# Optimization experiments

Measured on AMD Instinct MI355X. Metric: run time of the kernel, lower is better.

## Reference

```python
import jax, jax.numpy as jnp
import numpy as np
from jax import lax

B, N, F_IN, DIM = 128, 200, 200, 32
E_PER = 6400
K1, K2 = 100, 50
OUT = 2
BN_EPS = 1e-5


def setup_inputs():
    key = jax.random.key(0)
    ks = jax.random.split(key, 16)
    x = jax.random.normal(ks[0], (B * N, F_IN), jnp.float32)
    src = jax.random.randint(ks[1], (B, E_PER), 0, N)
    dst = jax.random.randint(ks[2], (B, E_PER), 0, N)
    off = (jnp.arange(B) * N)[:, None]
    edge_index = jnp.stack([(src + off).reshape(-1), (dst + off).reshape(-1)]).astype(jnp.int32)
    batch = jnp.repeat(jnp.arange(B, dtype=jnp.int32), N)

    def lin(k, i, o):
        kw, kb = jax.random.split(k)
        return (jax.random.normal(kw, (i, o), jnp.float32) / np.float32(np.sqrt(i)),
                jax.random.normal(kb, (o,), jnp.float32) * 0.01)

    w1a, b1a = lin(ks[3], F_IN, DIM)
    w1b, b1b = lin(ks[4], DIM, DIM)
    w2a, b2a = lin(ks[5], DIM, DIM)
    w2b, b2b = lin(ks[6], DIM, DIM)
    pw1 = jax.random.normal(ks[7], (DIM,), jnp.float32)
    pw2 = jax.random.normal(ks[8], (DIM,), jnp.float32)
    fc1_w, fc1_b = lin(ks[9], 2 * DIM, 4 * DIM)
    fc2_w, fc2_b = lin(ks[10], 4 * DIM, 8 * DIM)
    fc3_w, fc3_b = lin(ks[11], 8 * DIM, OUT)
    return dict(x=x, edge_index=edge_index, batch=batch,
                w1a=w1a, b1a=b1a, w1b=w1b, b1b=b1b,
                w2a=w2a, b2a=b2a, w2b=w2b, b2b=b2b,
                pw1=pw1, pw2=pw2,
                fc1_w=fc1_w, fc1_b=fc1_b, fc2_w=fc2_w, fc2_b=fc2_b,
                fc3_w=fc3_w, fc3_b=fc3_b,
                bn1_g=jnp.ones((4 * DIM,)), bn1_b=jnp.zeros((4 * DIM,)),
                bn1_m=jnp.zeros((4 * DIM,)), bn1_v=jnp.ones((4 * DIM,)),
                bn2_g=jnp.ones((8 * DIM,)), bn2_b=jnp.zeros((8 * DIM,)),
                bn2_m=jnp.zeros((8 * DIM,)), bn2_v=jnp.ones((8 * DIM,)))


def gin_conv(x, src, dst, valid, wa, ba, wb, bb, n_nodes):
    # PyG GINConv: mlp((1+eps)*x + sum_{j->i} x_j), eps=0 (default)
    msg = x[src]
    if valid is not None:
        msg = msg * valid[:, None]
    aggr = jax.ops.segment_sum(msg, dst, num_segments=n_nodes)
    h = jax.nn.relu((x + aggr) @ wa + ba)
    return h @ wb + bb


def topk_pool(x, src, dst, valid, pw, nb, n_per, k):
    # PyG TopKPooling: score = tanh((x.w)/||w||); keep top-k per graph; x <- x[perm]*score[perm]
    score = jnp.tanh((x @ pw) / jnp.linalg.norm(pw))
    topv, topi = lax.top_k(score.reshape(nb, n_per), k)  # [nb,k], descending (matches PyG ordering)
    perm = (topi + (jnp.arange(nb) * n_per)[:, None]).reshape(-1)
    x_new = x[perm] * topv.reshape(-1, 1)
    new_id = jnp.full((nb * n_per,), -1, jnp.int32).at[perm].set(jnp.arange(nb * k, dtype=jnp.int32))
    s, d = new_id[src], new_id[dst]
    v = (s >= 0) & (d >= 0)
    if valid is not None:
        v = v & valid
    return x_new, jnp.maximum(s, 0), jnp.maximum(d, 0), v, topv


def bn_eval(h, g, b, m, v):
    return (h - m) * lax.rsqrt(v + BN_EPS) * g + b


def reference(x, edge_index, batch,
              w1a, b1a, w1b, b1b, w2a, b2a, w2b, b2b, pw1, pw2,
              fc1_w, fc1_b, fc2_w, fc2_b, fc3_w, fc3_b,
              bn1_g, bn1_b, bn1_m, bn1_v, bn2_g, bn2_b, bn2_m, bn2_v):
    src, dst = edge_index[0], edge_index[1]
    h = jax.nn.relu(gin_conv(x, src, dst, None, w1a, b1a, w1b, b1b, B * N))
    h, src, dst, valid, attn1 = topk_pool(h, src, dst, None, pw1, B, N, K1)
    hb = h.reshape(B, K1, DIM)
    x1 = jnp.concatenate([hb.max(axis=1), hb.mean(axis=1)], axis=1)  # gmp || gap
    h = jax.nn.relu(gin_conv(h, src, dst, valid.astype(h.dtype), w2a, b2a, w2b, b2b, B * K1))
    h, src, dst, valid, attn2 = topk_pool(h, src, dst, valid, pw2, B, K1, K2)
    hb = h.reshape(B, K2, DIM)
    x2 = jnp.concatenate([hb.max(axis=1), hb.mean(axis=1)], axis=1)
    z = x1 + x2
    z = bn_eval(jax.nn.relu(z @ fc1_w + fc1_b), bn1_g, bn1_b, bn1_m, bn1_v)  # dropout p=0.6 inactive (eval)
    z = bn_eval(jax.nn.relu(z @ fc2_w + fc2_b), bn2_g, bn2_b, bn2_m, bn2_v)
    xy = jax.nn.log_softmax(z @ fc3_w + fc3_b, axis=-1)
    return xy, jax.nn.sigmoid(attn1), jax.nn.sigmoid(attn2)
```

## Files before the change

kernel.cpp:

```cpp
#include <hip/hip_runtime.h>
#include <math.h>

#define NGRAPH 128
#define NNODE  200
#define FIN    200
#define DIM    32
#define EPER   6400
#define ETOT   819200
#define KP1    100
#define KP2    50

#define W1B_OFF  0
#define W2A_OFF  1024
#define W2B_OFF  2048
#define B1A_OFF  3072
#define B1B_OFF  3104
#define B2A_OFF  3136
#define B2B_OFF  3168
#define PW1_OFF  3200
#define PW2_OFF  3232
#define NRM1_OFF 3264
#define NRM2_OFF 3265
#define SW_SIZE  3280

__device__ __forceinline__ int swz(int row, int chunk) {
  return (row << 5) + (((chunk ^ ((row >> 2) & 7))) << 2);
}

__global__ __launch_bounds__(256, 2) void proj_k(const float* __restrict__ x,
                                                 const float* __restrict__ w1a,
                                                 float* __restrict__ y) {
  __shared__ __align__(16) float sw[FIN * DIM];
  const int tid = threadIdx.x;
  for (int i = tid; i < FIN * DIM; i += 256) sw[i] = w1a[i];
  __syncthreads();
  if (tid >= 200) return;
  const int rg = tid >> 2, cg = tid & 3;
  const int d0 = cg * 8;
  const int r0 = blockIdx.x * 50 + rg;
  const float* x0 = x + (size_t)r0 * FIN;
  float a0[8] = {0, 0, 0, 0, 0, 0, 0, 0};
  for (int k = 0; k < FIN; k += 4) {
    const float4 xa = *(const float4*)&x0[k];
#pragma unroll
    for (int j = 0; j < 4; ++j) {
      const float4 wa = *(const float4*)&sw[(k + j) * DIM + d0];
      const float4 wb = *(const float4*)&sw[(k + j) * DIM + d0 + 4];
      const float s0 = (j == 0) ? xa.x : (j == 1) ? xa.y : (j == 2) ? xa.z : xa.w;
      a0[0] += s0 * wa.x; a0[1] += s0 * wa.y; a0[2] += s0 * wa.z; a0[3] += s0 * wa.w;
      a0[4] += s0 * wb.x; a0[5] += s0 * wb.y; a0[6] += s0 * wb.z; a0[7] += s0 * wb.w;
    }
  }
  float4 o;
  o.x = a0[0]; o.y = a0[1]; o.z = a0[2]; o.w = a0[3];
  *(float4*)&y[(size_t)r0 * 32 + d0] = o;
  o.x = a0[4]; o.y = a0[5]; o.z = a0[6]; o.w = a0[7];
  *(float4*)&y[(size_t)r0 * 32 + d0 + 4] = o;
}

template <int ROWS, bool RELU, bool BIAS, bool FUSE>
__device__ __forceinline__ void mm2r(const float* __restrict__ A,
                                     const float* __restrict__ A2,
                                     const float* __restrict__ fb,
                                     const float* __restrict__ W,
                                     float* __restrict__ O,
                                     const float* __restrict__ bias, int tid) {
  if (tid < ROWS * 2) {
    const int rg = tid >> 2, cg = tid & 3;
    const int r0 = rg * 2, d0 = cg * 8;
    float acc[2][8];
#pragma unroll
    for (int r = 0; r < 2; ++r)
#pragma unroll
      for (int c = 0; c < 8; ++c) acc[r][c] = 0.f;
#pragma unroll
    for (int kc = 0; kc < 8; ++kc) {
      float4 av[2];
#pragma unroll
      for (int r = 0; r < 2; ++r) {
        const int p = swz(r0 + r, kc);
        float4 v = *(const float4*)&A[p];
        if (FUSE) {
          const float4 u = *(const float4*)&A2[p];
          const float4 b = *(const float4*)&fb[kc * 4];
          v.x = fmaxf(v.x + u.x + b.x, 0.f);
          v.y = fmaxf(v.y + u.y + b.y, 0.f);
          v.z = fmaxf(v.z + u.z + b.z, 0.f);
          v.w = fmaxf(v.w + u.w + b.w, 0.f);
        }
        av[r] = v;
      }
#pragma unroll
      for (int j = 0; j < 4; ++j) {
        const int k = kc * 4 + j;
        const float4 wa = *(const float4*)&W[k * 32 + d0];
        const float4 wb = *(const float4*)&W[k * 32 + d0 + 4];
#pragma unroll
        for (int r = 0; r < 2; ++r) {
          const float xs = (j == 0) ? av[r].x : (j == 1) ? av[r].y
                                  : (j == 2) ? av[r].z : av[r].w;
          acc[r][0] += xs * wa.x; acc[r][1] += xs * wa.y;
          acc[r][2] += xs * wa.z; acc[r][3] += xs * wa.w;
          acc[r][4] += xs * wb.x; acc[r][5] += xs * wb.y;
          acc[r][6] += xs * wb.z; acc[r][7] += xs * wb.w;
        }
      }
    }
#pragma unroll
    for (int r = 0; r < 2; ++r) {
      float v[8];
#pragma unroll
      for (int c = 0; c < 8; ++c) {
        float t = acc[r][c];
        if (BIAS) t += bias[d0 + c];
        if (RELU) t = fmaxf(t, 0.f);
        v[c] = t;
      }
      float4 o0, o1;
      o0.x = v[0]; o0.y = v[1]; o0.z = v[2]; o0.w = v[3];
      o1.x = v[4]; o1.y = v[5]; o1.z = v[6]; o1.w = v[7];
      *(float4*)&O[swz(r0 + r, cg * 2)] = o0;
      *(float4*)&O[swz(r0 + r, cg * 2 + 1)] = o1;
    }
  }
}

__device__ __forceinline__ void scan_counts(const int* __restrict__ cnt,
                                            int* __restrict__ start, int lane) {
  const int b = lane * 4;
  const int c0 = (cnt[b + 0] + 3) & ~3;
  const int c1 = (cnt[b + 1] + 3) & ~3;
  const int c2 = (cnt[b + 2] + 3) & ~3;
  const int c3 = (cnt[b + 3] + 3) & ~3;
  const int t01 = c0 + c1;
  const int t012 = t01 + c2;
  const int tot = t012 + c3;
  int run = tot;
#pragma unroll
  for (int off = 1; off < 64; off <<= 1) {
    const int t = __shfl_up(run, off);
    if (lane >= off) run += t;
  }
  const int e = run - tot;
  start[b + 0] = e;
  start[b + 1] = e + c0;
  start[b + 2] = e + t01;
  start[b + 3] = e + t012;
}

template <int NN>
__device__ __forceinline__ void aggregate(const float* __restrict__ sYv,
                                          float* __restrict__ sAgv,
                                          const int* __restrict__ sSrcv,
                                          const int* __restrict__ sStartv,
                                          const int* __restrict__ sCntv, int tid) {
  const int slot = tid >> 3, part = tid & 7;
#pragma unroll
  for (int p = 0; p < (NN + 127) / 128; ++p) {
    const int n = p * 128 + slot;
    if (n < NN) {
      const int jb = sStartv[n];
      const int je = jb + sCntv[n];
      float4 a0 = {0, 0, 0, 0}, a1 = {0, 0, 0, 0}, a2 = {0, 0, 0, 0}, a3 = {0, 0, 0, 0};
      int j = jb;
      for (; j + 4 <= je; j += 4) {
        const int4 ss = *(const int4*)&sSrcv[j];
        const float4 v0 = *(const float4*)&sYv[swz(ss.x, part)];
        const float4 v1 = *(const float4*)&sYv[swz(ss.y, part)];
        const float4 v2 = *(const float4*)&sYv[swz(ss.z, part)];
        const float4 v3 = *(const float4*)&sYv[swz(ss.w, part)];
        a0.x += v0.x; a0.y += v0.y; a0.z += v0.z; a0.w += v0.w;
        a1.x += v1.x; a1.y += v1.y; a1.z += v1.z; a1.w += v1.w;
        a2.x += v2.x; a2.y += v2.y; a2.z += v2.z; a2.w += v2.w;
        a3.x += v3.x; a3.y += v3.y; a3.z += v3.z; a3.w += v3.w;
      }
      for (; j < je; ++j) {
        const float4 v = *(const float4*)&sYv[swz(sSrcv[j], part)];
        a0.x += v.x; a0.y += v.y; a0.z += v.z; a0.w += v.w;
      }
      float4 o;
      o.x = (a0.x + a1.x) + (a2.x + a3.x);
      o.y = (a0.y + a1.y) + (a2.y + a3.y);
      o.z = (a0.z + a1.z) + (a2.z + a3.z);
      o.w = (a0.w + a1.w) + (a2.w + a3.w);
      *(float4*)&sAgv[swz(n, part)] = o;
    }
  }
}

__global__ __launch_bounds__(1024, 1) void gin_rest(
    const float* __restrict__ y1g_all, const int* __restrict__ ei,
    const float* __restrict__ b1a, const float* __restrict__ w1b,
    const float* __restrict__ b1b, const float* __restrict__ w2a,
    const float* __restrict__ b2a, const float* __restrict__ w2b,
    const float* __restrict__ b2b, const float* __restrict__ pw1,
    const float* __restrict__ pw2,
    const float* __restrict__ fc1w, const float* __restrict__ fc1b,
    const float* __restrict__ fc2w, const float* __restrict__ fc2b,
    const float* __restrict__ fc3w, const float* __restrict__ fc3b,
    const float* __restrict__ bn1g, const float* __restrict__ bn1b,
    const float* __restrict__ bn1m, const float* __restrict__ bn1v,
    const float* __restrict__ bn2g, const float* __restrict__ bn2b,
    const float* __restrict__ bn2m, const float* __restrict__ bn2v,
    float* __restrict__ out) {
  __shared__ __align__(16) float sY[6400];
  __shared__ __align__(16) float sAg[6400];
  __shared__ __align__(16) float sH[6400];
  __shared__ __align__(16) float sHp[3200];
  __shared__ __align__(16) float sW[SW_SIZE];
  __shared__ __align__(16) int sSrc[7040];
  __shared__ unsigned short sEdge[6400];
  __shared__ int sCnt[256], sStart[256], sOfs[256];
  __shared__ int sCnt2[256], sStart2[256], sOfs2[256];
  __shared__ float sScore[256];
  __shared__ int sNewid[256];
  __shared__ float sZ[64];
  __shared__ float sZ1[128];
  __shared__ float sZ2[256];
  __shared__ float sLg[2];

  const int tid = threadIdx.x;
  const int g = blockIdx.x;

  if (tid < 512) {
    if (tid < 256) { sCnt[tid] = 0; sOfs[tid] = 0; }
    const float* yg = y1g_all + (size_t)g * (NNODE * DIM);
    for (int i = tid; i < 1600; i += 512) {
      const float4 v = *(const float4*)&yg[i * 4];
      *(float4*)&sY[swz(i >> 3, i & 7)] = v;
    }
    for (int i = tid; i < 1024; i += 512) {
      sW[W1B_OFF + i] = w1b[i];
      sW[W2A_OFF + i] = w2a[i];
      sW[W2B_OFF + i] = w2b[i];
    }
    if (tid < 32) {
      sW[B1A_OFF + tid] = b1a[tid];
      sW[B1B_OFF + tid] = b1b[tid];
      sW[B2A_OFF + tid] = b2a[tid];
      sW[B2B_OFF + tid] = b2b[tid];
      sW[PW1_OFF + tid] = pw1[tid];
      sW[PW2_OFF + tid] = pw2[tid];
    }
  } else {
    const int eb = g * EPER, nb = g * NNODE;
    for (int i = tid - 512; i < EPER / 4; i += 512) {
      const int4 ss = *(const int4*)&ei[eb + i * 4];
      const int4 dd = *(const int4*)&ei[ETOT + eb + i * 4];
      sEdge[i * 4 + 0] = (unsigned short)(((ss.x - nb) << 8) | (dd.x - nb));
      sEdge[i * 4 + 1] = (unsigned short)(((ss.y - nb) << 8) | (dd.y - nb));
      sEdge[i * 4 + 2] = (unsigned short)(((ss.z - nb) << 8) | (dd.z - nb));
      sEdge[i * 4 + 3] = (unsigned short)(((ss.w - nb) << 8) | (dd.w - nb));
    }
  }
  __syncthreads();

  if (tid == 0) {
    float s = 0.f;
    for (int k = 0; k < 32; ++k) s += sW[PW1_OFF + k] * sW[PW1_OFF + k];
    sW[NRM1_OFF] = sqrtf(s);
  } else if (tid == 1) {
    float s = 0.f;
    for (int k = 0; k < 32; ++k) s += sW[PW2_OFF + k] * sW[PW2_OFF + k];
    sW[NRM2_OFF] = sqrtf(s);
  }
  if (tid < 800) {
    const uint4 u = *(const uint4*)&sEdge[tid * 8];
    atomicAdd(&sCnt[u.x & 255], 1);
    atomicAdd(&sCnt[(u.x >> 16) & 255], 1);
    atomicAdd(&sCnt[u.y & 255], 1);
    atomicAdd(&sCnt[(u.y >> 16) & 255], 1);
    atomicAdd(&sCnt[u.z & 255], 1);
    atomicAdd(&sCnt[(u.z >> 16) & 255], 1);
    atomicAdd(&sCnt[u.w & 255], 1);
    atomicAdd(&sCnt[(u.w >> 16) & 255], 1);
  }
  __syncthreads();

  if (tid < 64) scan_counts(sCnt, sStart, tid);
  __syncthreads();

  for (int e = tid; e < EPER; e += 1024) {
    const unsigned short p = sEdge[e];
    sSrc[sStart[p & 255] + atomicAdd(&sOfs[p & 255], 1)] = p >> 8;
  }
  __syncthreads();

  aggregate<NNODE>(sY, sAg, sSrc, sStart, sCnt, tid);
  __syncthreads();

  mm2r<200, true, true, true>(sY, sAg, &sW[B1A_OFF], &sW[W1B_OFF], sH,
                              &sW[B1B_OFF], tid);
  if (tid >= 512) {
    const int i = tid - 512;
    if (i < 256) sCnt2[i] = 0;
    else if (i < 512) sOfs2[i - 256] = 0;
  }
  __syncthreads();

  if (tid < NNODE) {
    float dot = 0.f;
#pragma unroll
    for (int kc = 0; kc < 8; ++kc) {
      const float4 v = *(const float4*)&sH[swz(tid, kc)];
      const float4 w = *(const float4*)&sW[PW1_OFF + kc * 4];
      dot += v.x * w.x + v.y * w.y + v.z * w.z + v.w * w.w;
    }
    sScore[tid] = tanhf(dot / sW[NRM1_OFF]);
  }
  __syncthreads();

  if (tid < NNODE * 4) {
    const int n = tid >> 2, q = tid & 3;
    const float s = sScore[n];
    int r = 0;
    for (int m = q * 50; m < q * 50 + 50; ++m) {
      const float sm = sScore[m];
      r += (sm > s) || (sm == s && m < n);
    }
    r += __shfl_xor(r, 1);
    r += __shfl_xor(r, 2);
    if (q == 0) {
      sNewid[n] = (r < KP1) ? r : -1;
      if (r < KP1) out[2 * NGRAPH + g * KP1 + r] = 1.f / (1.f + expf(-s));
    }
  }
  __syncthreads();

  if (tid < 400) {
    const int n = tid >> 1, kb = (tid & 1) * 4;
    const int r = sNewid[n];
    if (r >= 0) {
      const float sc = sScore[n];
#pragma unroll
      for (int k = 0; k < 4; ++k) {
        float4 v = *(const float4*)&sH[swz(n, kb + k)];
        v.x *= sc; v.y *= sc; v.z *= sc; v.w *= sc;
        *(float4*)&sHp[swz(r, kb + k)] = v;
      }
    }
  } else if (tid >= 512) {
    for (int e = tid - 512; e < EPER; e += 512) {
      const unsigned short p = sEdge[e];
      const int s1 = sNewid[p >> 8], d1 = sNewid[p & 255];
      if (s1 >= 0 && d1 >= 0) atomicAdd(&sCnt2[d1], 1);
    }
  }
  __syncthreads();

  if (tid < 32) {
    const int ch = tid >> 2, w = tid & 3;
    float m0 = -INFINITY, m1 = -INFINITY, s0 = 0.f, s1 = 0.f;
    for (int r = 0; r < KP1; r += 2) {
      const float v0 = sHp[swz(r, ch) + w];
      const float v1 = sHp[swz(r + 1, ch) + w];
      m0 = fmaxf(m0, v0); m1 = fmaxf(m1, v1);
      s0 += v0; s1 += v1;
    }
    sZ[tid] = fmaxf(m0, m1);
    sZ[32 + tid] = (s0 + s1) / (float)KP1;
  } else if (tid >= 64 && tid < 128) {
    scan_counts(sCnt2, sStart2, tid - 64);
  }
  __syncthreads();

  mm2r<KP1, false, false, false>(sHp, nullptr, nullptr, &sW[W2A_OFF], sY,
                                 nullptr, tid);
  if (tid >= 256) {
    for (int e = tid - 256; e < EPER; e += 768) {
      const unsigned short p = sEdge[e];
      const int s1 = sNewid[p >> 8], d1 = sNewid[p & 255];
      if (s1 >= 0 && d1 >= 0)
        sSrc[sStart2[d1] + atomicAdd(&sOfs2[d1], 1)] = s1;
    }
  }
  __syncthreads();

  aggregate<KP1>(sY, sAg, sSrc, sStart2, sCnt2, tid);
  __syncthreads();

  mm2r<KP1, true, true, true>(sY, sAg, &sW[B2A_OFF], &sW[W2B_OFF], sH,
                              &sW[B2B_OFF], tid);
  __syncthreads();

  if (tid < KP1) {
    float dot = 0.f;
#pragma unroll
    for (int kc = 0; kc < 8; ++kc) {
      const float4 v = *(const float4*)&sH[swz(tid, kc)];
      const float4 w = *(const float4*)&sW[PW2_OFF + kc * 4];
      dot += v.x * w.x + v.y * w.y + v.z * w.z + v.w * w.w;
    }
    sScore[tid] = tanhf(dot / sW[NRM2_OFF]);
  }
  __syncthreads();

  if (tid < KP1 * 4) {
    const int n = tid >> 2, q = tid & 3;
    const float s = sScore[n];
    int r = 0;
    for (int m = q * 25; m < q * 25 + 25; ++m) {
      const float sm = sScore[m];
      r += (sm > s) || (sm == s && m < n);
    }
    r += __shfl_xor(r, 1);
    r += __shfl_xor(r, 2);
    if (q == 0) {
      sNewid[n] = (r < KP2) ? r : -1;
      if (r < KP2)
        out[2 * NGRAPH + NGRAPH * KP1 + g * KP2 + r] = 1.f / (1.f + expf(-s));
    }
  }
  __syncthreads();

  if (tid < 200) {
    const int n = tid >> 1, kb = (tid & 1) * 4;
    const int r = sNewid[n];
    if (r >= 0) {
      const float sc = sScore[n];
#pragma unroll
      for (int k = 0; k < 4; ++k) {
        float4 v = *(const float4*)&sH[swz(n, kb + k)];
        v.x *= sc; v.y *= sc; v.z *= sc; v.w *= sc;
        *(float4*)&sHp[swz(r, kb + k)] = v;
      }
    }
  }
  __syncthreads();

  if (tid < 32) {
    const int ch = tid >> 2, w = tid & 3;
    float m0 = -INFINITY, m1 = -INFINITY, s0 = 0.f, s1 = 0.f;
    for (int r = 0; r < KP2; r += 2) {
      const float v0 = sHp[swz(r, ch) + w];
      const float v1 = sHp[swz(r + 1, ch) + w];
      m0 = fmaxf(m0, v0); m1 = fmaxf(m1, v1);
      s0 += v0; s1 += v1;
    }
    sZ[tid] += fmaxf(m0, m1);
    sZ[32 + tid] += (s0 + s1) / (float)KP2;
  }
  __syncthreads();

  if (tid < 128) {
    float a = fc1b[tid];
    for (int k = 0; k < 64; ++k) a += sZ[k] * fc1w[k * 128 + tid];
    a = fmaxf(a, 0.f);
    a = (a - bn1m[tid]) * rsqrtf(bn1v[tid] + 1e-5f) * bn1g[tid] + bn1b[tid];
    sZ1[tid] = a;
  }
  __syncthreads();

  if (tid < 256) {
    float a = fc2b[tid];
    for (int k = 0; k < 128; ++k) a += sZ1[k] * fc2w[k * 256 + tid];
    a = fmaxf(a, 0.f);
    a = (a - bn2m[tid]) * rsqrtf(bn2v[tid] + 1e-5f) * bn2g[tid] + bn2b[tid];
    sZ2[tid] = a;
  }
  __syncthreads();

  if (tid < 128) {
    const int o = tid >> 6, lane = tid & 63;
    float a = 0.f;
    for (int k = lane; k < 256; k += 64) a += sZ2[k] * fc3w[k * 2 + o];
#pragma unroll
    for (int off = 32; off; off >>= 1) a += __shfl_down(a, off);
    if (lane == 0) sLg[o] = a + fc3b[o];
  }
  __syncthreads();

  if (tid == 0) {
    const float l0 = sLg[0], l1 = sLg[1];
    const float m = fmaxf(l0, l1);
    const float lse = m + logf(expf(l0 - m) + expf(l1 - m));
    out[g * 2 + 0] = l0 - lse;
    out[g * 2 + 1] = l1 - lse;
  }
}

extern "C" void kernel_launch(void* const* d_in, const int* in_sizes, int n_in,
                              void* d_out, int out_size, void* d_ws,
                              size_t ws_size, hipStream_t stream) {
  (void)in_sizes; (void)n_in; (void)out_size; (void)ws_size;
  float* y1 = (float*)d_ws;
  proj_k<<<512, 256, 0, stream>>>((const float*)d_in[0],
                                  (const float*)d_in[3], y1);
  gin_rest<<<NGRAPH, 1024, 0, stream>>>(
      y1, (const int*)d_in[1],
      (const float*)d_in[4],
      (const float*)d_in[5], (const float*)d_in[6],
      (const float*)d_in[7], (const float*)d_in[8],
      (const float*)d_in[9], (const float*)d_in[10],
      (const float*)d_in[11], (const float*)d_in[12],
      (const float*)d_in[13], (const float*)d_in[14],
      (const float*)d_in[15], (const float*)d_in[16],
      (const float*)d_in[17], (const float*)d_in[18],
      (const float*)d_in[19], (const float*)d_in[20],
      (const float*)d_in[21], (const float*)d_in[22],
      (const float*)d_in[23], (const float*)d_in[24],
      (const float*)d_in[25], (const float*)d_in[26],
      (float*)d_out);
}
```

Before: 52.21 us.

## Fuse input projection into per-graph kernel and overlap edge sorting via LDS flags

```diff
diff --git a/kernel.cpp b/kernel.cpp
--- a/kernel.cpp
+++ b/kernel.cpp
@@ -27,44 +27,20 @@
   return (row << 5) + (((chunk ^ ((row >> 2) & 7))) << 2);
 }
 
-__global__ __launch_bounds__(256, 2) void proj_k(const float* __restrict__ x,
-                                                 const float* __restrict__ w1a,
-                                                 float* __restrict__ y) {
-  __shared__ __align__(16) float sw[FIN * DIM];
-  const int tid = threadIdx.x;
-  for (int i = tid; i < FIN * DIM; i += 256) sw[i] = w1a[i];
-  __syncthreads();
-  if (tid >= 200) return;
-  const int rg = tid >> 2, cg = tid & 3;
-  const int d0 = cg * 8;
-  const int r0 = blockIdx.x * 50 + rg;
-  const float* x0 = x + (size_t)r0 * FIN;
-  float a0[8] = {0, 0, 0, 0, 0, 0, 0, 0};
-  for (int k = 0; k < FIN; k += 4) {
-    const float4 xa = *(const float4*)&x0[k];
-#pragma unroll
-    for (int j = 0; j < 4; ++j) {
-      const float4 wa = *(const float4*)&sw[(k + j) * DIM + d0];
-      const float4 wb = *(const float4*)&sw[(k + j) * DIM + d0 + 4];
-      const float s0 = (j == 0) ? xa.x : (j == 1) ? xa.y : (j == 2) ? xa.z : xa.w;
-      a0[0] += s0 * wa.x; a0[1] += s0 * wa.y; a0[2] += s0 * wa.z; a0[3] += s0 * wa.w;
-      a0[4] += s0 * wb.x; a0[5] += s0 * wb.y; a0[6] += s0 * wb.z; a0[7] += s0 * wb.w;
-    }
-  }
-  float4 o;
-  o.x = a0[0]; o.y = a0[1]; o.z = a0[2]; o.w = a0[3];
-  *(float4*)&y[(size_t)r0 * 32 + d0] = o;
-  o.x = a0[4]; o.y = a0[5]; o.z = a0[6]; o.w = a0[7];
-  *(float4*)&y[(size_t)r0 * 32 + d0 + 4] = o;
-}
-
-template <int ROWS, bool RELU, bool BIAS, bool FUSE>
+__device__ __forceinline__ void lds_spin(volatile int* f, int target) {
+  while (*f != target) __builtin_amdgcn_s_sleep(2);
+}
+
+template <int ROWS, bool RELU, bool BIAS, bool FUSE, bool SCORE>
 __device__ __forceinline__ void mm2r(const float* __restrict__ A,
                                      const float* __restrict__ A2,
                                      const float* __restrict__ fb,
                                      const float* __restrict__ W,
                                      float* __restrict__ O,
-                                     const float* __restrict__ bias, int tid) {
+                                     const float* __restrict__ bias,
+                                     const float* __restrict__ pw,
+                                     const float* __restrict__ nrmp,
+                                     float* __restrict__ scoreOut, int tid) {
   if (tid < ROWS * 2) {
     const int rg = tid >> 2, cg = tid & 3;
     const int r0 = rg * 2, d0 = cg * 8;
@@ -106,6 +82,7 @@
         }
       }
     }
+    float dot[2] = {0.f, 0.f};
 #pragma unroll
     for (int r = 0; r < 2; ++r) {
       float v[8];
@@ -116,11 +93,26 @@
         if (RELU) t = fmaxf(t, 0.f);
         v[c] = t;
       }
+      if (SCORE) {
+        float d = 0.f;
+#pragma unroll
+        for (int c = 0; c < 8; ++c) d += v[c] * pw[d0 + c];
+        dot[r] = d;
+      }
       float4 o0, o1;
       o0.x = v[0]; o0.y = v[1]; o0.z = v[2]; o0.w = v[3];
       o1.x = v[4]; o1.y = v[5]; o1.z = v[6]; o1.w = v[7];
       *(float4*)&O[swz(r0 + r, cg * 2)] = o0;
       *(float4*)&O[swz(r0 + r, cg * 2 + 1)] = o1;
+    }
+    if (SCORE) {
+      dot[0] += __shfl_xor(dot[0], 1); dot[0] += __shfl_xor(dot[0], 2);
+      dot[1] += __shfl_xor(dot[1], 1); dot[1] += __shfl_xor(dot[1], 2);
+      if ((tid & 3) == 0) {
+        const float nrm = *nrmp;
+        scoreOut[r0] = tanhf(dot[0] / nrm);
+        scoreOut[r0 + 1] = tanhf(dot[1] / nrm);
+      }
     }
   }
 }
@@ -188,13 +180,13 @@
   }
 }
 
-__global__ __launch_bounds__(1024, 1) void gin_rest(
-    const float* __restrict__ y1g_all, const int* __restrict__ ei,
-    const float* __restrict__ b1a, const float* __restrict__ w1b,
-    const float* __restrict__ b1b, const float* __restrict__ w2a,
-    const float* __restrict__ b2a, const float* __restrict__ w2b,
-    const float* __restrict__ b2b, const float* __restrict__ pw1,
-    const float* __restrict__ pw2,
+__global__ __launch_bounds__(1024, 1) void gin_fused(
+    const float* __restrict__ x, const int* __restrict__ ei,
+    const float* __restrict__ w1a, const float* __restrict__ b1a,
+    const float* __restrict__ w1b, const float* __restrict__ b1b,
+    const float* __restrict__ w2a, const float* __restrict__ b2a,
+    const float* __restrict__ w2b, const float* __restrict__ b2b,
+    const float* __restrict__ pw1, const float* __restrict__ pw2,
     const float* __restrict__ fc1w, const float* __restrict__ fc1b,
     const float* __restrict__ fc2w, const float* __restrict__ fc2b,
     const float* __restrict__ fc3w, const float* __restrict__ fc3b,
@@ -212,6 +204,7 @@
   __shared__ unsigned short sEdge[6400];
   __shared__ int sCnt[256], sStart[256], sOfs[256];
   __shared__ int sCnt2[256], sStart2[256], sOfs2[256];
+  __shared__ int sFlag[4];
   __shared__ float sScore[256];
   __shared__ int sNewid[256];
   __shared__ float sZ[64];
@@ -222,18 +215,9 @@
   const int tid = threadIdx.x;
   const int g = blockIdx.x;
 
-  if (tid < 512) {
-    if (tid < 256) { sCnt[tid] = 0; sOfs[tid] = 0; }
-    const float* yg = y1g_all + (size_t)g * (NNODE * DIM);
-    for (int i = tid; i < 1600; i += 512) {
-      const float4 v = *(const float4*)&yg[i * 4];
-      *(float4*)&sY[swz(i >> 3, i & 7)] = v;
-    }
-    for (int i = tid; i < 1024; i += 512) {
-      sW[W1B_OFF + i] = w1b[i];
-      sW[W2A_OFF + i] = w2a[i];
-      sW[W2B_OFF + i] = w2b[i];
-    }
+  if (tid < 256) {
+    for (int i = tid; i < 1600; i += 256)
+      *(float4*)&sAg[i * 4] = ((const float4*)w1a)[i];
     if (tid < 32) {
       sW[B1A_OFF + tid] = b1a[tid];
       sW[B1B_OFF + tid] = b1b[tid];
@@ -242,6 +226,21 @@
       sW[PW1_OFF + tid] = pw1[tid];
       sW[PW2_OFF + tid] = pw2[tid];
     }
+  } else if (tid < 512) {
+    const int t = tid - 256;
+    for (int i = t; i < 768; i += 256) {
+      const float4 v = (i < 256) ? ((const float4*)w1b)[i]
+                    : (i < 512) ? ((const float4*)w2a)[i - 256]
+                                : ((const float4*)w2b)[i - 512];
+      const int off = (i < 256) ? W1B_OFF + i * 4
+                    : (i < 512) ? W2A_OFF + (i - 256) * 4
+                                : W2B_OFF + (i - 512) * 4;
+      *(float4*)&sW[off] = v;
+    }
+    for (int i = t; i < 256; i += 256) {
+      sCnt[i] = 0; sOfs[i] = 0; sCnt2[i] = 0; sOfs2[i] = 0;
+    }
+    if (t < 4) sFlag[t] = 0;
   } else {
     const int eb = g * EPER, nb = g * NNODE;
     for (int i = tid - 512; i < EPER / 4; i += 512) {
@@ -255,59 +254,79 @@
   }
   __syncthreads();
 
-  if (tid == 0) {
+  if (tid < 200) {
+    const int rg = tid >> 2, cg = tid & 3;
+    const int n0 = rg * 4, d0 = cg * 8;
+    float acc[4][8];
+#pragma unroll
+    for (int r = 0; r < 4; ++r)
+#pragma unroll
+      for (int c = 0; c < 8; ++c) acc[r][c] = 0.f;
+    const float* xg = x + ((size_t)g * NNODE + n0) * FIN;
+    for (int k = 0; k < FIN; k += 4) {
+      float4 xv[4];
+#pragma unroll
+      for (int r = 0; r < 4; ++r)
+        xv[r] = *(const float4*)&xg[r * FIN + k];
+#pragma unroll
+      for (int j = 0; j < 4; ++j) {
+        const float4 wa = *(const float4*)&sAg[(k + j) * 32 + d0];
+        const float4 wb = *(const float4*)&sAg[(k + j) * 32 + d0 + 4];
+#pragma unroll
+        for (int r = 0; r < 4; ++r) {
+          const float xs = (j == 0) ? xv[r].x : (j == 1) ? xv[r].y
+                                   : (j == 2) ? xv[r].z : xv[r].w;
+          acc[r][0] += xs * wa.x; acc[r][1] += xs * wa.y;
+          acc[r][2] += xs * wa.z; acc[r][3] += xs * wa.w;
+          acc[r][4] += xs * wb.x; acc[r][5] += xs * wb.y;
+          acc[r][6] += xs * wb.z; acc[r][7] += xs * wb.w;
+        }
+      }
+    }
+#pragma unroll
+    for (int r = 0; r < 4; ++r) {
+      float4 o0, o1;
+      o0.x = acc[r][0]; o0.y = acc[r][1]; o0.z = acc[r][2]; o0.w = acc[r][3];
+      o1.x = acc[r][4]; o1.y = acc[r][5]; o1.z = acc[r][6]; o1.w = acc[r][7];
+      *(float4*)&sY[swz(n0 + r, cg * 2)] = o0;
+      *(float4*)&sY[swz(n0 + r, cg * 2 + 1)] = o1;
+    }
+  } else if (tid == 200) {
     float s = 0.f;
     for (int k = 0; k < 32; ++k) s += sW[PW1_OFF + k] * sW[PW1_OFF + k];
     sW[NRM1_OFF] = sqrtf(s);
-  } else if (tid == 1) {
+  } else if (tid == 201) {
     float s = 0.f;
     for (int k = 0; k < 32; ++k) s += sW[PW2_OFF + k] * sW[PW2_OFF + k];
     sW[NRM2_OFF] = sqrtf(s);
-  }
-  if (tid < 800) {
-    const uint4 u = *(const uint4*)&sEdge[tid * 8];
-    atomicAdd(&sCnt[u.x & 255], 1);
-    atomicAdd(&sCnt[(u.x >> 16) & 255], 1);
-    atomicAdd(&sCnt[u.y & 255], 1);
-    atomicAdd(&sCnt[(u.y >> 16) & 255], 1);
-    atomicAdd(&sCnt[u.z & 255], 1);
-    atomicAdd(&sCnt[(u.z >> 16) & 255], 1);
-    atomicAdd(&sCnt[u.w & 255], 1);
-    atomicAdd(&sCnt[(u.w >> 16) & 255], 1);
-  }
-  __syncthreads();
-
-  if (tid < 64) scan_counts(sCnt, sStart, tid);
-  __syncthreads();
-
-  for (int e = tid; e < EPER; e += 1024) {
-    const unsigned short p = sEdge[e];
-    sSrc[sStart[p & 255] + atomicAdd(&sOfs[p & 255], 1)] = p >> 8;
+  } else if (tid >= 256) {
+    const int t = tid - 256;
+    for (int e = t; e < EPER; e += 768)
+      atomicAdd(&sCnt[sEdge[e] & 255], 1);
+    __threadfence_block();
+    atomicAdd(&sFlag[0], 1);
+    if (tid >= 960) {
+      lds_spin(&sFlag[0], 768);
+      __threadfence_block();
+      scan_counts(sCnt, sStart, tid - 960);
+      __threadfence_block();
+      if (tid == 960) atomicExch(&sFlag[1], 1);
+    }
+    lds_spin(&sFlag[1], 1);
+    __threadfence_block();
+    for (int e = t; e < EPER; e += 768) {
+      const unsigned short p = sEdge[e];
+      sSrc[sStart[p & 255] + atomicAdd(&sOfs[p & 255], 1)] = p >> 8;
+    }
   }
   __syncthreads();
 
   aggregate<NNODE>(sY, sAg, sSrc, sStart, sCnt, tid);
   __syncthreads();
 
-  mm2r<200, true, true, true>(sY, sAg, &sW[B1A_OFF], &sW[W1B_OFF], sH,
-                              &sW[B1B_OFF], tid);
-  if (tid >= 512) {
-    const int i = tid - 512;
-    if (i < 256) sCnt2[i] = 0;
-    else if (i < 512) sOfs2[i - 256] = 0;
-  }
-  __syncthreads();
-
-  if (tid < NNODE) {
-    float dot = 0.f;
-#pragma unroll
-    for (int kc = 0; kc < 8; ++kc) {
-      const float4 v = *(const float4*)&sH[swz(tid, kc)];
-      const float4 w = *(const float4*)&sW[PW1_OFF + kc * 4];
-      dot += v.x * w.x + v.y * w.y + v.z * w.z + v.w * w.w;
-    }
-    sScore[tid] = tanhf(dot / sW[NRM1_OFF]);
-  }
+  mm2r<200, true, true, true, true>(sY, sAg, &sW[B1A_OFF], &sW[W1B_OFF], sH,
+                                    &sW[B1B_OFF], &sW[PW1_OFF], &sW[NRM1_OFF],
+                                    sScore, tid);
   __syncthreads();
 
   if (tid < NNODE * 4) {
@@ -324,32 +343,24 @@
       sNewid[n] = (r < KP1) ? r : -1;
       if (r < KP1) out[2 * NGRAPH + g * KP1 + r] = 1.f / (1.f + expf(-s));
     }
-  }
-  __syncthreads();
-
-  if (tid < 400) {
-    const int n = tid >> 1, kb = (tid & 1) * 4;
-    const int r = sNewid[n];
-    if (r >= 0) {
-      const float sc = sScore[n];
-#pragma unroll
-      for (int k = 0; k < 4; ++k) {
-        float4 v = *(const float4*)&sH[swz(n, kb + k)];
-        v.x *= sc; v.y *= sc; v.z *= sc; v.w *= sc;
-        *(float4*)&sHp[swz(r, kb + k)] = v;
-      }
-    }
-  } else if (tid >= 512) {
-    for (int e = tid - 512; e < EPER; e += 512) {
-      const unsigned short p = sEdge[e];
-      const int s1 = sNewid[p >> 8], d1 = sNewid[p & 255];
-      if (s1 >= 0 && d1 >= 0) atomicAdd(&sCnt2[d1], 1);
-    }
-  }
-  __syncthreads();
-
-  if (tid < 32) {
-    const int ch = tid >> 2, w = tid & 3;
+    if (r < KP1) {
+#pragma unroll
+      for (int c = 0; c < 2; ++c) {
+        const int ch = q * 2 + c;
+        float4 v = *(const float4*)&sH[swz(n, ch)];
+        v.x *= s; v.y *= s; v.z *= s; v.w *= s;
+        *(float4*)&sHp[swz(r, ch)] = v;
+      }
+    }
+  }
+  __syncthreads();
+
+  mm2r<KP1, false, false, false, false>(sHp, nullptr, nullptr, &sW[W2A_OFF],
+                                        sY, nullptr, nullptr, nullptr, nullptr,
+                                        tid);
+  if (tid >= 256 && tid < 288) {
+    const int t = tid - 256;
+    const int ch = t >> 2, w = t & 3;
     float m0 = -INFINITY, m1 = -INFINITY, s0 = 0.f, s1 = 0.f;
     for (int r = 0; r < KP1; r += 2) {
       const float v0 = sHp[swz(r, ch) + w];
@@ -357,17 +368,27 @@
       m0 = fmaxf(m0, v0); m1 = fmaxf(m1, v1);
       s0 += v0; s1 += v1;
     }
-    sZ[tid] = fmaxf(m0, m1);
-    sZ[32 + tid] = (s0 + s1) / (float)KP1;
-  } else if (tid >= 64 && tid < 128) {
-    scan_counts(sCnt2, sStart2, tid - 64);
-  }
-  __syncthreads();
-
-  mm2r<KP1, false, false, false>(sHp, nullptr, nullptr, &sW[W2A_OFF], sY,
-                                 nullptr, tid);
-  if (tid >= 256) {
-    for (int e = tid - 256; e < EPER; e += 768) {
+    sZ[t] = fmaxf(m0, m1);
+    sZ[32 + t] = (s0 + s1) / (float)KP1;
+  } else if (tid >= 512) {
+    const int t = tid - 512;
+    for (int e = t; e < EPER; e += 512) {
+      const unsigned short p = sEdge[e];
+      const int s1 = sNewid[p >> 8], d1 = sNewid[p & 255];
+      if (s1 >= 0 && d1 >= 0) atomicAdd(&sCnt2[d1], 1);
+    }
+    __threadfence_block();
+    atomicAdd(&sFlag[2], 1);
+    if (tid >= 960) {
+      lds_spin(&sFlag[2], 512);
+      __threadfence_block();
+      scan_counts(sCnt2, sStart2, tid - 960);
+      __threadfence_block();
+      if (tid == 960) atomicExch(&sFlag[3], 1);
+    }
+    lds_spin(&sFlag[3], 1);
+    __threadfence_block();
+    for (int e = t; e < EPER; e += 512) {
       const unsigned short p = sEdge[e];
       const int s1 = sNewid[p >> 8], d1 = sNewid[p & 255];
       if (s1 >= 0 && d1 >= 0)
@@ -379,20 +400,9 @@
   aggregate<KP1>(sY, sAg, sSrc, sStart2, sCnt2, tid);
   __syncthreads();
 
-  mm2r<KP1, true, true, true>(sY, sAg, &sW[B2A_OFF], &sW[W2B_OFF], sH,
-                              &sW[B2B_OFF], tid);
-  __syncthreads();
-
-  if (tid < KP1) {
-    float dot = 0.f;
-#pragma unroll
-    for (int kc = 0; kc < 8; ++kc) {
-      const float4 v = *(const float4*)&sH[swz(tid, kc)];
-      const float4 w = *(const float4*)&sW[PW2_OFF + kc * 4];
-      dot += v.x * w.x + v.y * w.y + v.z * w.z + v.w * w.w;
-    }
-    sScore[tid] = tanhf(dot / sW[NRM2_OFF]);
-  }
+  mm2r<KP1, true, true, true, true>(sY, sAg, &sW[B2A_OFF], &sW[W2B_OFF], sH,
+                                    &sW[B2B_OFF], &sW[PW2_OFF], &sW[NRM2_OFF],
+                                    sScore, tid);
   __syncthreads();
 
   if (tid < KP1 * 4) {
@@ -410,19 +420,13 @@
       if (r < KP2)
         out[2 * NGRAPH + NGRAPH * KP1 + g * KP2 + r] = 1.f / (1.f + expf(-s));
     }
-  }
-  __syncthreads();
-
-  if (tid < 200) {
-    const int n = tid >> 1, kb = (tid & 1) * 4;
-    const int r = sNewid[n];
-    if (r >= 0) {
-      const float sc = sScore[n];
-#pragma unroll
-      for (int k = 0; k < 4; ++k) {
-        float4 v = *(const float4*)&sH[swz(n, kb + k)];
-        v.x *= sc; v.y *= sc; v.z *= sc; v.w *= sc;
-        *(float4*)&sHp[swz(r, kb + k)] = v;
+    if (r < KP2) {
+#pragma unroll
+      for (int c = 0; c < 2; ++c) {
+        const int ch = q * 2 + c;
+        float4 v = *(const float4*)&sH[swz(n, ch)];
+        v.x *= s; v.y *= s; v.z *= s; v.w *= s;
+        *(float4*)&sHp[swz(r, ch)] = v;
       }
     }
   }
@@ -442,53 +446,66 @@
   }
   __syncthreads();
 
-  if (tid < 128) {
-    float a = fc1b[tid];
-    for (int k = 0; k < 64; ++k) a += sZ[k] * fc1w[k * 128 + tid];
-    a = fmaxf(a, 0.f);
-    a = (a - bn1m[tid]) * rsqrtf(bn1v[tid] + 1e-5f) * bn1g[tid] + bn1b[tid];
-    sZ1[tid] = a;
-  }
-  __syncthreads();
-
-  if (tid < 256) {
-    float a = fc2b[tid];
-    for (int k = 0; k < 128; ++k) a += sZ1[k] * fc2w[k * 256 + tid];
-    a = fmaxf(a, 0.f);
-    a = (a - bn2m[tid]) * rsqrtf(bn2v[tid] + 1e-5f) * bn2g[tid] + bn2b[tid];
-    sZ2[tid] = a;
-  }
-  __syncthreads();
-
-  if (tid < 128) {
-    const int o = tid >> 6, lane = tid & 63;
+  if (tid < 512) {
+    const int o = tid >> 2, q = tid & 3;
     float a = 0.f;
-    for (int k = lane; k < 256; k += 64) a += sZ2[k] * fc3w[k * 2 + o];
-#pragma unroll
-    for (int off = 32; off; off >>= 1) a += __shfl_down(a, off);
-    if (lane == 0) sLg[o] = a + fc3b[o];
-  }
-  __syncthreads();
-
-  if (tid == 0) {
-    const float l0 = sLg[0], l1 = sLg[1];
-    const float m = fmaxf(l0, l1);
-    const float lse = m + logf(expf(l0 - m) + expf(l1 - m));
-    out[g * 2 + 0] = l0 - lse;
-    out[g * 2 + 1] = l1 - lse;
+    for (int k = q * 16; k < q * 16 + 16; ++k) a += sZ[k] * fc1w[k * 128 + o];
+    a += __shfl_xor(a, 1);
+    a += __shfl_xor(a, 2);
+    if (q == 0) {
+      a += fc1b[o];
+      a = fmaxf(a, 0.f);
+      a = (a - bn1m[o]) * rsqrtf(bn1v[o] + 1e-5f) * bn1g[o] + bn1b[o];
+      sZ1[o] = a;
+    }
+  }
+  __syncthreads();
+
+  if (tid < 512) {
+    const int o = tid >> 1, h = tid & 1;
+    float a = 0.f;
+    for (int k = h * 64; k < h * 64 + 64; ++k) a += sZ1[k] * fc2w[k * 256 + o];
+    a += __shfl_xor(a, 1);
+    if (h == 0) {
+      a += fc2b[o];
+      a = fmaxf(a, 0.f);
+      a = (a - bn2m[o]) * rsqrtf(bn2v[o] + 1e-5f) * bn2g[o] + bn2b[o];
+      sZ2[o] = a;
+    }
+  }
+  __syncthreads();
+
+  if (tid < 64) {
+    const int k4 = tid * 4;
+    float a0 = 0.f, a1 = 0.f;
+#pragma unroll
+    for (int k = 0; k < 4; ++k) {
+      const float z = sZ2[k4 + k];
+      a0 += z * fc3w[(k4 + k) * 2 + 0];
+      a1 += z * fc3w[(k4 + k) * 2 + 1];
+    }
+#pragma unroll
+    for (int off = 32; off; off >>= 1) {
+      a0 += __shfl_xor(a0, off);
+      a1 += __shfl_xor(a1, off);
+    }
+    if (tid == 0) {
+      const float l0 = a0 + fc3b[0], l1 = a1 + fc3b[1];
+      const float m = fmaxf(l0, l1);
+      const float lse = m + logf(expf(l0 - m) + expf(l1 - m));
+      out[g * 2 + 0] = l0 - lse;
+      out[g * 2 + 1] = l1 - lse;
+    }
   }
 }
 
 extern "C" void kernel_launch(void* const* d_in, const int* in_sizes, int n_in,
                               void* d_out, int out_size, void* d_ws,
                               size_t ws_size, hipStream_t stream) {
-  (void)in_sizes; (void)n_in; (void)out_size; (void)ws_size;
-  float* y1 = (float*)d_ws;
-  proj_k<<<512, 256, 0, stream>>>((const float*)d_in[0],
-                                  (const float*)d_in[3], y1);
-  gin_rest<<<NGRAPH, 1024, 0, stream>>>(
-      y1, (const int*)d_in[1],
-      (const float*)d_in[4],
+  (void)in_sizes; (void)n_in; (void)out_size; (void)d_ws; (void)ws_size;
+  gin_fused<<<NGRAPH, 1024, 0, stream>>>(
+      (const float*)d_in[0], (const int*)d_in[1],
+      (const float*)d_in[3], (const float*)d_in[4],
       (const float*)d_in[5], (const float*)d_in[6],
       (const float*)d_in[7], (const float*)d_in[8],
       (const float*)d_in[9], (const float*)d_in[10],
```

Result: no change. 52.75 us (+1.0%).
